# Kernel optimization log

Hardware: AMD Instinct MI355X
Metric: run time of the kernel (lower is better)

## Reference

```python
import jax, jax.numpy as jnp
import numpy as np

N = 20000          # nodes
E = 320000         # edges (avg degree 16)
HID = 256          # hidden_size
HEADS = 8          # num_heads
HD = HID // HEADS  # head_dim = 32


def setup_inputs() -> dict:
    key = jax.random.key(0)
    ks = jax.random.split(key, 12)
    scale = 1.0 / np.sqrt(HID).astype(np.float32)
    def lin_w(k):
        return jax.random.normal(k, (HID, HID), jnp.float32) * scale
    def lin_b(k):
        return jax.random.normal(k, (HID,), jnp.float32) * 0.01
    return {
        "h":   jax.random.normal(ks[0], (N, HID), jnp.float32),
        "Wq": lin_w(ks[1]), "bq": lin_b(ks[2]),
        "Wk": lin_w(ks[3]), "bk": lin_b(ks[4]),
        "Wv": lin_w(ks[5]), "bv": lin_b(ks[6]),
        "Wo": lin_w(ks[7]), "bo": lin_b(ks[8]),
        "rows": jax.random.randint(ks[9],  (E,), 0, N),  # dst/query node of each edge
        "cols": jax.random.randint(ks[10], (E,), 0, N),  # src/key node of each edge
    }


def reference(h, Wq, bq, Wk, bk, Wv, bv, Wo, bo, rows, cols):
    n = h.shape[0]
    scaling = HD ** (-0.5)
    # projections; reshape exactly as torch: (N, head_dim, num_heads)
    q = ((h @ Wq) + bq).reshape(n, HD, HEADS) * scaling
    k = ((h @ Wk) + bk).reshape(n, HD, HEADS)
    v = ((h @ Wv) + bv).reshape(n, HD, HEADS)
    # bsddmm: per-edge, per-head score s[e,h] = sum_d q[rows[e],d,h] * k[cols[e],d,h]
    s = jnp.einsum("edh,edh->eh", q[rows], k[cols])  # [E, HEADS]
    # sparse row-wise softmax (over each row's edges)
    m = jax.ops.segment_max(s, rows, num_segments=n)          # [N, HEADS]
    e = jnp.exp(s - m[rows])                                   # [E, HEADS]
    z = jax.ops.segment_sum(e, rows, num_segments=n)           # [N, HEADS]
    attn = e / z[rows]                                          # [E, HEADS]
    # bspmm: out[i,d,h] = sum_{e: rows[e]=i} attn[e,h] * v[cols[e],d,h]
    out = jax.ops.segment_sum(attn[:, None, :] * v[cols], rows, num_segments=n)  # [N, HD, HEADS]
    return out.reshape(n, -1) @ Wo + bo
```

## Files before the change

### kernel.cpp

```cpp
#include <hip/hip_runtime.h>
#include <hip/hip_bf16.h>
#include <math.h>

#define NNODES 20000
#define NEDGES 320000
#define SCAT_BLOCKS 1250
#define MBLK 313

using f32x4 = __attribute__((ext_vector_type(4))) float;
using s16x8 = __attribute__((ext_vector_type(8))) short;
using u16x8 = __attribute__((ext_vector_type(8))) unsigned short;

__device__ __forceinline__ float bf2f(unsigned short u) {
    union { unsigned int i; float f; } c; c.i = ((unsigned int)u) << 16; return c.f;
}
__device__ __forceinline__ unsigned short f2bf(float f) {
    __hip_bfloat16 h = __float2bfloat16(f);
    return *reinterpret_cast<unsigned short*>(&h);
}
__device__ __forceinline__ u16x8 packA(const float4& x, const float4& y) {
    u16x8 u; u[0]=f2bf(x.x); u[1]=f2bf(x.y); u[2]=f2bf(x.z); u[3]=f2bf(x.w);
             u[4]=f2bf(y.x); u[5]=f2bf(y.y); u[6]=f2bf(y.z); u[7]=f2bf(y.w);
    return u;
}
template <int CTRL>
__device__ __forceinline__ float dpp_xadd(float x) {
    union { float f; int i; } a, b;
    a.f = x;
    b.i = __builtin_amdgcn_update_dpp(0, a.i, CTRL, 0xf, 0xf, true);
    return x + b.f;
}

__global__ __launch_bounds__(256) void prep_hist_k(
    const float* __restrict__ Wq, const float* __restrict__ bq,
    const float* __restrict__ Wk, const float* __restrict__ bk,
    const float* __restrict__ Wv, const float* __restrict__ bv,
    const float* __restrict__ Wo, const int* __restrict__ rows,
    unsigned short* __restrict__ wt, float* __restrict__ bp,
    int* __restrict__ counts)
{
    const int gid = blockIdx.x * 256 + threadIdx.x;
    const float SCQ = 0.17677669529663687f * 1.4426950408889634f;
    if (gid < 262144) {
        const int mat = gid >> 16, r = gid & 65535;
        if (mat < 3) {
            const int k = r >> 8, c = r & 255;
            const int n_old = ((c & 31) << 3) | (c >> 5);
            const float* W = (mat == 0) ? Wq : (mat == 1) ? Wk : Wv;
            float val = W[k * 256 + n_old];
            if (mat == 0) val *= SCQ;
            wt[mat * 65536 + c * 256 + k] = f2bf(val);
        } else {
            const int c = r >> 8, n = r & 255;
            const int n_old = ((c & 31) << 3) | (c >> 5);
            wt[3 * 65536 + n * 256 + c] = f2bf(Wo[n_old * 256 + n]);
        }
    } else if (gid < 262912) {
        const int idx = gid - 262144;
        const int mat = idx >> 8, c = idx & 255;
        const int n_old = ((c & 31) << 3) | (c >> 5);
        const float* b = (mat == 0) ? bq : (mat == 1) ? bk : bv;
        float val = b[n_old];
        if (mat == 0) val *= SCQ;
        bp[mat * 256 + c] = val;
    } else if (gid < 262912 + NEDGES) {
        atomicAdd(&counts[rows[gid - 262912]], 1);
    }
}

__global__ __launch_bounds__(1024) void scan_k(const int* __restrict__ counts,
                                               int* __restrict__ row_start)
{
    __shared__ int wsum[16];
    const int t = threadIdx.x, lane = t & 63, w = t >> 6;
    const int base = t * 20;
    int c[20]; int s = 0;
    #pragma unroll
    for (int j = 0; j < 20; ++j) {
        const int idx = base + j;
        c[j] = (idx < NNODES) ? counts[idx] : 0;
        s += c[j];
    }
    int incl = s;
    #pragma unroll
    for (int off = 1; off < 64; off <<= 1) {
        const int y = __shfl_up(incl, off);
        if (lane >= off) incl += y;
    }
    if (lane == 63) wsum[w] = incl;
    __syncthreads();
    int prev = 0;
    for (int i = 0; i < w; ++i) prev += wsum[i];
    int run = prev + incl - s;
    if (t == 0) row_start[0] = 0;
    #pragma unroll
    for (int j = 0; j < 20; ++j) {
        const int idx = base + j;
        run += c[j];
        if (idx < NNODES) row_start[idx + 1] = run;
    }
}

__global__ __launch_bounds__(256) void qkv_scatter_k(
    const float* __restrict__ h,
    const unsigned short* __restrict__ wt, const float* __restrict__ bp,
    const int* __restrict__ rows, const int* __restrict__ cols,
    const int* __restrict__ row_start, int* __restrict__ cursor,
    int* __restrict__ cols_sorted,
    unsigned short* __restrict__ qo, unsigned short* __restrict__ kv)
{
    const int t = threadIdx.x;
    if (blockIdx.x < SCAT_BLOCKS) {
        const int i = blockIdx.x * 256 + t;
        if (i < NEDGES) {
            const int r = rows[i];
            const int pos = row_start[r] + atomicAdd(&cursor[r], 1);
            cols_sorted[pos] = cols[i];
        }
        return;
    }
    const int bid = blockIdx.x - SCAT_BLOCKS;
    const int mat = bid / MBLK;
    const int bm = (bid % MBLK) * 64;
    const unsigned short* W = wt + mat * 65536;

    __shared__ __align__(16) unsigned short As[64][264];

    const int lane = t & 63, w = t >> 6;
    const int wc = w * 64;
    const int l15 = lane & 15, l4 = lane >> 4;

    u16x8 breg[4][8];
    #pragma unroll
    for (int nt = 0; nt < 4; ++nt)
        #pragma unroll
        for (int k8 = 0; k8 < 8; ++k8)
            breg[nt][k8] = *(const u16x8*)&W[(wc + nt * 16 + l15) * 256 + k8 * 32 + l4 * 8];

    {
        const int arow = t >> 2, acoff = (t & 3) * 8;
        const int m0 = min(bm + arow, NNODES - 1);
        const float* ph = h + m0 * 256 + acoff;
        #pragma unroll
        for (int s = 0; s < 8; ++s) {
            const float4 fa = *(const float4*)(ph + s * 32);
            const float4 fb = *(const float4*)(ph + s * 32 + 4);
            *(u16x8*)&As[arow][acoff + s * 32] = packA(fa, fb);
        }
    }
    __syncthreads();

    f32x4 acc[4][4];
    #pragma unroll
    for (int i = 0; i < 4; ++i)
        #pragma unroll
        for (int j = 0; j < 4; ++j) acc[i][j] = (f32x4){0.f, 0.f, 0.f, 0.f};

    #pragma unroll
    for (int k8 = 0; k8 < 8; ++k8) {
        s16x8 a[4];
        const int kk = k8 * 32 + l4 * 8;
        #pragma unroll
        for (int i = 0; i < 4; ++i)
            a[i] = *(const s16x8*)&As[i * 16 + l15][kk];
        #pragma unroll
        for (int i = 0; i < 4; ++i)
            #pragma unroll
            for (int j = 0; j < 4; ++j)
                acc[i][j] = __builtin_amdgcn_mfma_f32_16x16x32_bf16(
                    a[i], (s16x8)breg[j][k8], acc[i][j], 0, 0, 0);
    }

    #pragma unroll
    for (int j = 0; j < 4; ++j) {
        const int n = wc + j * 16 + l15;
        const float bval = bp[mat * 256 + n];
        const int kvb = ((n >> 3) << 4) + (n & 7) + ((mat == 2) ? 8 : 0);
        #pragma unroll
        for (int i = 0; i < 4; ++i) {
            #pragma unroll
            for (int r = 0; r < 4; ++r) {
                const int m = bm + i * 16 + l4 * 4 + r;
                if (m < NNODES) {
                    const unsigned short val = f2bf(acc[i][j][r] + bval);
                    if (mat == 0) qo[m * 256 + n] = val;
                    else          kv[m * 512 + kvb] = val;
                }
            }
        }
    }
}

__global__ __launch_bounds__(256) void out_proj_k(
    const unsigned short* __restrict__ A,
    const unsigned short* __restrict__ wt, const float* __restrict__ bo,
    float* __restrict__ C)
{
    const int t = threadIdx.x;
    const int bm = blockIdx.x * 64;
    const unsigned short* W = wt + 3 * 65536;

    __shared__ __align__(16) unsigned short As[64][264];

    const int lane = t & 63, w = t >> 6;
    const int wc = w * 64;
    const int l15 = lane & 15, l4 = lane >> 4;

    u16x8 breg[4][8];
    #pragma unroll
    for (int nt = 0; nt < 4; ++nt)
        #pragma unroll
        for (int k8 = 0; k8 < 8; ++k8)
            breg[nt][k8] = *(const u16x8*)&W[(wc + nt * 16 + l15) * 256 + k8 * 32 + l4 * 8];

    {
        const int arow = t >> 2, acoff = (t & 3) * 8;
        const int m0 = min(bm + arow, NNODES - 1);
        const unsigned short* pa = A + m0 * 256 + acoff;
        #pragma unroll
        for (int s = 0; s < 8; ++s)
            *(u16x8*)&As[arow][acoff + s * 32] = *(const u16x8*)(pa + s * 32);
    }
    __syncthreads();

    f32x4 acc[4][4];
    #pragma unroll
    for (int i = 0; i < 4; ++i)
        #pragma unroll
        for (int j = 0; j < 4; ++j) acc[i][j] = (f32x4){0.f, 0.f, 0.f, 0.f};

    #pragma unroll
    for (int k8 = 0; k8 < 8; ++k8) {
        s16x8 a[4];
        const int kk = k8 * 32 + l4 * 8;
        #pragma unroll
        for (int i = 0; i < 4; ++i)
            a[i] = *(const s16x8*)&As[i * 16 + l15][kk];
        #pragma unroll
        for (int i = 0; i < 4; ++i)
            #pragma unroll
            for (int j = 0; j < 4; ++j)
                acc[i][j] = __builtin_amdgcn_mfma_f32_16x16x32_bf16(
                    a[i], (s16x8)breg[j][k8], acc[i][j], 0, 0, 0);
    }

    #pragma unroll
    for (int j = 0; j < 4; ++j) {
        const int n = wc + j * 16 + l15;
        const float bval = bo[n];
        #pragma unroll
        for (int i = 0; i < 4; ++i) {
            #pragma unroll
            for (int r = 0; r < 4; ++r) {
                const int m = bm + i * 16 + l4 * 4 + r;
                if (m < NNODES) C[m * 256 + n] = acc[i][j][r] + bval;
            }
        }
    }
}

__global__ __launch_bounds__(256) void row_attn_k(
    const unsigned short* __restrict__ q, const unsigned short* __restrict__ kv,
    const int* __restrict__ row_start, const int* __restrict__ cols_sorted,
    unsigned short* __restrict__ ot)
{
    const int lane = threadIdx.x & 63;
    const int w5 = lane & 31;
    const int half = lane >> 5;
    const int row = __builtin_amdgcn_readfirstlane(blockIdx.x * 4 + (threadIdx.x >> 6));
    const int rs = row_start[row];
    const int re = row_start[row + 1];
    const int deg = re - rs;

    float qd[8];
    {
        const u16x8 qu = *reinterpret_cast<const u16x8*>(&q[row * 256 + w5 * 8]);
        #pragma unroll
        for (int d = 0; d < 8; ++d) qd[d] = bf2f(qu[d]);
    }
    float o[8] = {0.f, 0.f, 0.f, 0.f, 0.f, 0.f, 0.f, 0.f};
    float z = 0.f;
    const int* cp = cols_sorted + rs;

#define LP(K, V, base) do { \
    const int c0 = cp[min((base), deg - 1)]; \
    const int c1 = cp[min((base) + 1, deg - 1)]; \
    const int cn = half ? c1 : c0; \
    const unsigned short* p_ = kv + cn * 512 + w5 * 16; \
    K = *reinterpret_cast<const u16x8*>(p_); \
    V = *reinterpret_cast<const u16x8*>(p_ + 8); \
} while (0)

#define CMP(K, V, base) do { \
    float pa_ = qd[0] * bf2f(K[0]); \
    float pb_ = qd[1] * bf2f(K[1]); \
    pa_ = fmaf(qd[2], bf2f(K[2]), pa_); \
    pb_ = fmaf(qd[3], bf2f(K[3]), pb_); \
    pa_ = fmaf(qd[4], bf2f(K[4]), pa_); \
    pb_ = fmaf(qd[5], bf2f(K[5]), pb_); \
    pa_ = fmaf(qd[6], bf2f(K[6]), pa_); \
    pb_ = fmaf(qd[7], bf2f(K[7]), pb_); \
    float p_ = pa_ + pb_; \
    p_ = dpp_xadd<0xB1>(p_); \
    p_ = dpp_xadd<0x4E>(p_); \
    const float e_ = ((base) + half < deg) ? exp2f(p_) : 0.f; \
    z += e_; \
    o[0] = fmaf(e_, bf2f(V[0]), o[0]); \
    o[1] = fmaf(e_, bf2f(V[1]), o[1]); \
    o[2] = fmaf(e_, bf2f(V[2]), o[2]); \
    o[3] = fmaf(e_, bf2f(V[3]), o[3]); \
    o[4] = fmaf(e_, bf2f(V[4]), o[4]); \
    o[5] = fmaf(e_, bf2f(V[5]), o[5]); \
    o[6] = fmaf(e_, bf2f(V[6]), o[6]); \
    o[7] = fmaf(e_, bf2f(V[7]), o[7]); \
} while (0)

    if (deg > 0) {
        u16x8 ak0, av0, ak1, av1, bk0, bv0, bk1, bv1;
        LP(ak0, av0, 0);
        LP(ak1, av1, 2);
        for (int i0 = 0; i0 < deg; i0 += 8) {
            const bool hb = (i0 + 4) < deg;
            if (hb) { LP(bk0, bv0, i0 + 4); LP(bk1, bv1, i0 + 6); }
            CMP(ak0, av0, i0);
            CMP(ak1, av1, i0 + 2);
            if (i0 + 8 < deg) { LP(ak0, av0, i0 + 8); LP(ak1, av1, i0 + 10); }
            if (hb) { CMP(bk0, bv0, i0 + 4); CMP(bk1, bv1, i0 + 6); }
        }
    }
#undef LP
#undef CMP

    z += __shfl_xor(z, 32);
    #pragma unroll
    for (int d = 0; d < 8; ++d) o[d] += __shfl_xor(o[d], 32);

    if (half == 0) {
        u16x8 r;
        if (deg > 0) {
            const float iz = 1.0f / z;
            #pragma unroll
            for (int d = 0; d < 8; ++d) r[d] = f2bf(o[d] * iz);
        } else {
            #pragma unroll
            for (int d = 0; d < 8; ++d) r[d] = 0;
        }
        *reinterpret_cast<u16x8*>(&ot[row * 256 + w5 * 8]) = r;
    }
}

extern "C" void kernel_launch(void* const* d_in, const int* in_sizes, int n_in,
                              void* d_out, int out_size, void* d_ws, size_t ws_size,
                              hipStream_t stream)
{
    const float* h  = (const float*)d_in[0];
    const float* Wq = (const float*)d_in[1];
    const float* bq = (const float*)d_in[2];
    const float* Wk = (const float*)d_in[3];
    const float* bk = (const float*)d_in[4];
    const float* Wv = (const float*)d_in[5];
    const float* bv = (const float*)d_in[6];
    const float* Wo = (const float*)d_in[7];
    const float* bo = (const float*)d_in[8];
    const int* rows = (const int*)d_in[9];
    const int* cols = (const int*)d_in[10];
    float* outp = (float*)d_out;

    char* ws = (char*)d_ws;
    unsigned short* q_b  = (unsigned short*)(ws + 0);
    unsigned short* kv_b = (unsigned short*)(ws + 10240000);
    unsigned short* ot_b = (unsigned short*)(ws + 30720000);
    unsigned short* wt   = (unsigned short*)(ws + 40960000);
    float* bp            = (float*)(ws + 41484288);
    int* row_start       = (int*)(ws + 41487360);
    int* counts          = (int*)(ws + 41567488);
    int* cursor          = (int*)(ws + 41647488);
    int* cols_sorted     = (int*)(ws + 41727488);

    hipMemsetAsync(ws + 41567488, 0, 160000, stream);

    prep_hist_k<<<2277, 256, 0, stream>>>(Wq, bq, Wk, bk, Wv, bv, Wo, rows,
                                          wt, bp, counts);
    scan_k<<<1, 1024, 0, stream>>>(counts, row_start);
    qkv_scatter_k<<<SCAT_BLOCKS + 3 * MBLK, 256, 0, stream>>>(
        h, wt, bp, rows, cols, row_start, cursor, cols_sorted, q_b, kv_b);
    row_attn_k<<<5000, 256, 0, stream>>>(q_b, kv_b, row_start, cols_sorted, ot_b);
    out_proj_k<<<MBLK, 256, 0, stream>>>(ot_b, wt, bo, outp);
}
```

Before: 237.1 us.

## Pre-convert h to bf16, retile weights into k-blocked layout, split K/V buffers

The prep kernel now also converts h to bf16 and writes the weights in a k-chunked [mat][k/32][n][32] layout. The GEMM kernels then stream B fragments from global memory per k-step instead of preloading 32 registers of B, which cuts register pressure, and they copy bf16 A tiles directly. K and V are stored in separate 256-wide buffers instead of one interleaved 512-wide buffer, so the attention kernel issues two separate gathers per edge. The cost is an extra 10 MB bf16 write and read of h, plus a shared GEMM body helper.

```diff
diff --git a/kernel.cpp b/kernel.cpp
--- a/kernel.cpp
+++ b/kernel.cpp
@@ -17,11 +17,6 @@
 __device__ __forceinline__ unsigned short f2bf(float f) {
     __hip_bfloat16 h = __float2bfloat16(f);
     return *reinterpret_cast<unsigned short*>(&h);
-}
-__device__ __forceinline__ u16x8 packA(const float4& x, const float4& y) {
-    u16x8 u; u[0]=f2bf(x.x); u[1]=f2bf(x.y); u[2]=f2bf(x.z); u[3]=f2bf(x.w);
-             u[4]=f2bf(y.x); u[5]=f2bf(y.y); u[6]=f2bf(y.z); u[7]=f2bf(y.w);
-    return u;
 }
 template <int CTRL>
 __device__ __forceinline__ float dpp_xadd(float x) {
@@ -31,13 +26,14 @@
     return x + b.f;
 }
 
-__global__ __launch_bounds__(256) void prep_hist_k(
+__global__ __launch_bounds__(256) void prep_all_k(
     const float* __restrict__ Wq, const float* __restrict__ bq,
     const float* __restrict__ Wk, const float* __restrict__ bk,
     const float* __restrict__ Wv, const float* __restrict__ bv,
     const float* __restrict__ Wo, const int* __restrict__ rows,
-    unsigned short* __restrict__ wt, float* __restrict__ bp,
-    int* __restrict__ counts)
+    const float* __restrict__ h,
+    unsigned short* __restrict__ wt2, float* __restrict__ bp,
+    int* __restrict__ counts, unsigned short* __restrict__ hb)
 {
     const int gid = blockIdx.x * 256 + threadIdx.x;
     const float SCQ = 0.17677669529663687f * 1.4426950408889634f;
@@ -49,11 +45,11 @@
             const float* W = (mat == 0) ? Wq : (mat == 1) ? Wk : Wv;
             float val = W[k * 256 + n_old];
             if (mat == 0) val *= SCQ;
-            wt[mat * 65536 + c * 256 + k] = f2bf(val);
+            wt2[((mat * 8 + (k >> 5)) * 256 + c) * 32 + (k & 31)] = f2bf(val);
         } else {
-            const int c = r >> 8, n = r & 255;
-            const int n_old = ((c & 31) << 3) | (c >> 5);
-            wt[3 * 65536 + n * 256 + c] = f2bf(Wo[n_old * 256 + n]);
+            const int k = r & 255, n = r >> 8;
+            const int n_old = ((k & 31) << 3) | (k >> 5);
+            wt2[((24 + (k >> 5)) * 256 + n) * 32 + (k & 31)] = f2bf(Wo[n_old * 256 + n]);
         }
     } else if (gid < 262912) {
         const int idx = gid - 262144;
@@ -63,8 +59,14 @@
         float val = b[n_old];
         if (mat == 0) val *= SCQ;
         bp[mat * 256 + c] = val;
-    } else if (gid < 262912 + NEDGES) {
+    } else if (gid < 582912) {
         atomicAdd(&counts[rows[gid - 262912]], 1);
+    } else {
+        const int i = (gid - 582912) * 4;
+        const float4 f = *reinterpret_cast<const float4*>(&h[i]);
+        ushort4 u;
+        u.x = f2bf(f.x); u.y = f2bf(f.y); u.z = f2bf(f.z); u.w = f2bf(f.w);
+        *reinterpret_cast<ushort4*>(&hb[i]) = u;
     }
 }
 
@@ -101,13 +103,58 @@
     }
 }
 
+__device__ __forceinline__ void gemm_body(
+    const unsigned short* __restrict__ Asrc,
+    const unsigned short* __restrict__ wt2, int mat, int bm,
+    f32x4 (&acc)[4][4], unsigned short (&As)[64][264],
+    int t, int lane)
+{
+    const int l15 = lane & 15, l4 = lane >> 4;
+    const int w = t >> 6;
+    const int wc = w * 64;
+    {
+        const int arow = t >> 2;
+        const int coff = (t & 3) * 64;
+        const int m0 = min(bm + arow, NNODES - 1);
+        const unsigned short* pa = Asrc + m0 * 256 + coff;
+        #pragma unroll
+        for (int s = 0; s < 8; ++s)
+            *(u16x8*)&As[arow][coff + s * 8] = *(const u16x8*)(pa + s * 8);
+    }
+    __syncthreads();
+
+    #pragma unroll
+    for (int i = 0; i < 4; ++i)
+        #pragma unroll
+        for (int j = 0; j < 4; ++j) acc[i][j] = (f32x4){0.f, 0.f, 0.f, 0.f};
+
+    const unsigned short* bb = wt2 + (mat * 8) * 256 * 32 + l4 * 8;
+    #pragma unroll
+    for (int k8 = 0; k8 < 8; ++k8) {
+        s16x8 b[4], a[4];
+        #pragma unroll
+        for (int j = 0; j < 4; ++j)
+            b[j] = *(const s16x8*)(bb + (k8 * 256 + wc + j * 16 + l15) * 32);
+        const int kk = k8 * 32 + l4 * 8;
+        #pragma unroll
+        for (int i = 0; i < 4; ++i)
+            a[i] = *(const s16x8*)&As[i * 16 + l15][kk];
+        #pragma unroll
+        for (int i = 0; i < 4; ++i)
+            #pragma unroll
+            for (int j = 0; j < 4; ++j)
+                acc[i][j] = __builtin_amdgcn_mfma_f32_16x16x32_bf16(a[i], b[j], acc[i][j], 0, 0, 0);
+    }
+}
+
 __global__ __launch_bounds__(256) void qkv_scatter_k(
-    const float* __restrict__ h,
-    const unsigned short* __restrict__ wt, const float* __restrict__ bp,
+    const unsigned short* __restrict__ hb,
+    const unsigned short* __restrict__ wt2, const float* __restrict__ bp,
     const int* __restrict__ rows, const int* __restrict__ cols,
     const int* __restrict__ row_start, int* __restrict__ cursor,
     int* __restrict__ cols_sorted,
-    unsigned short* __restrict__ qo, unsigned short* __restrict__ kv)
+    unsigned short* __restrict__ qo, unsigned short* __restrict__ ko,
+    unsigned short* __restrict__ vo)
 {
     const int t = threadIdx.x;
     if (blockIdx.x < SCAT_BLOCKS) {
@@ -119,73 +166,28 @@
         }
         return;
     }
-    const int bid = blockIdx.x - SCAT_BLOCKS;
-    const int mat = bid / MBLK;
-    const int bm = (bid % MBLK) * 64;
-    const unsigned short* W = wt + mat * 65536;
+    const int gb = blockIdx.x - SCAT_BLOCKS;
+    const int mat = gb / MBLK;
+    const int bm = (gb % MBLK) * 64;
+    unsigned short* outp = (mat == 0) ? qo : (mat == 1) ? ko : vo;
 
     __shared__ __align__(16) unsigned short As[64][264];
-
-    const int lane = t & 63, w = t >> 6;
-    const int wc = w * 64;
+    const int lane = t & 63;
+    f32x4 acc[4][4];
+    gemm_body(hb, wt2, mat, bm, acc, As, t, lane);
+
     const int l15 = lane & 15, l4 = lane >> 4;
-
-    u16x8 breg[4][8];
-    #pragma unroll
-    for (int nt = 0; nt < 4; ++nt)
-        #pragma unroll
-        for (int k8 = 0; k8 < 8; ++k8)
-            breg[nt][k8] = *(const u16x8*)&W[(wc + nt * 16 + l15) * 256 + k8 * 32 + l4 * 8];
-
-    {
-        const int arow = t >> 2, acoff = (t & 3) * 8;
-        const int m0 = min(bm + arow, NNODES - 1);
-        const float* ph = h + m0 * 256 + acoff;
-        #pragma unroll
-        for (int s = 0; s < 8; ++s) {
-            const float4 fa = *(const float4*)(ph + s * 32);
-            const float4 fb = *(const float4*)(ph + s * 32 + 4);
-            *(u16x8*)&As[arow][acoff + s * 32] = packA(fa, fb);
-        }
-    }
-    __syncthreads();
-
-    f32x4 acc[4][4];
-    #pragma unroll
-    for (int i = 0; i < 4; ++i)
-        #pragma unroll
-        for (int j = 0; j < 4; ++j) acc[i][j] = (f32x4){0.f, 0.f, 0.f, 0.f};
-
-    #pragma unroll
-    for (int k8 = 0; k8 < 8; ++k8) {
-        s16x8 a[4];
-        const int kk = k8 * 32 + l4 * 8;
-        #pragma unroll
-        for (int i = 0; i < 4; ++i)
-            a[i] = *(const s16x8*)&As[i * 16 + l15][kk];
-        #pragma unroll
-        for (int i = 0; i < 4; ++i)
-            #pragma unroll
-            for (int j = 0; j < 4; ++j)
-                acc[i][j] = __builtin_amdgcn_mfma_f32_16x16x32_bf16(
-                    a[i], (s16x8)breg[j][k8], acc[i][j], 0, 0, 0);
-    }
-
+    const int wc = (t >> 6) * 64;
     #pragma unroll
     for (int j = 0; j < 4; ++j) {
         const int n = wc + j * 16 + l15;
         const float bval = bp[mat * 256 + n];
-        const int kvb = ((n >> 3) << 4) + (n & 7) + ((mat == 2) ? 8 : 0);
         #pragma unroll
         for (int i = 0; i < 4; ++i) {
             #pragma unroll
             for (int r = 0; r < 4; ++r) {
                 const int m = bm + i * 16 + l4 * 4 + r;
-                if (m < NNODES) {
-                    const unsigned short val = f2bf(acc[i][j][r] + bval);
-                    if (mat == 0) qo[m * 256 + n] = val;
-                    else          kv[m * 512 + kvb] = val;
-                }
+                if (m < NNODES) outp[m * 256 + n] = f2bf(acc[i][j][r] + bval);
             }
         }
     }
@@ -193,57 +195,19 @@
 
 __global__ __launch_bounds__(256) void out_proj_k(
     const unsigned short* __restrict__ A,
-    const unsigned short* __restrict__ wt, const float* __restrict__ bo,
+    const unsigned short* __restrict__ wt2, const float* __restrict__ bo,
     float* __restrict__ C)
 {
     const int t = threadIdx.x;
     const int bm = blockIdx.x * 64;
-    const unsigned short* W = wt + 3 * 65536;
 
     __shared__ __align__(16) unsigned short As[64][264];
-
-    const int lane = t & 63, w = t >> 6;
-    const int wc = w * 64;
+    const int lane = t & 63;
+    f32x4 acc[4][4];
+    gemm_body(A, wt2, 3, bm, acc, As, t, lane);
+
     const int l15 = lane & 15, l4 = lane >> 4;
-
-    u16x8 breg[4][8];
-    #pragma unroll
-    for (int nt = 0; nt < 4; ++nt)
-        #pragma unroll
-        for (int k8 = 0; k8 < 8; ++k8)
-            breg[nt][k8] = *(const u16x8*)&W[(wc + nt * 16 + l15) * 256 + k8 * 32 + l4 * 8];
-
-    {
-        const int arow = t >> 2, acoff = (t & 3) * 8;
-        const int m0 = min(bm + arow, NNODES - 1);
-        const unsigned short* pa = A + m0 * 256 + acoff;
-        #pragma unroll
-        for (int s = 0; s < 8; ++s)
-            *(u16x8*)&As[arow][acoff + s * 32] = *(const u16x8*)(pa + s * 32);
-    }
-    __syncthreads();
-
-    f32x4 acc[4][4];
-    #pragma unroll
-    for (int i = 0; i < 4; ++i)
-        #pragma unroll
-        for (int j = 0; j < 4; ++j) acc[i][j] = (f32x4){0.f, 0.f, 0.f, 0.f};
-
-    #pragma unroll
-    for (int k8 = 0; k8 < 8; ++k8) {
-        s16x8 a[4];
-        const int kk = k8 * 32 + l4 * 8;
-        #pragma unroll
-        for (int i = 0; i < 4; ++i)
-            a[i] = *(const s16x8*)&As[i * 16 + l15][kk];
-        #pragma unroll
-        for (int i = 0; i < 4; ++i)
-            #pragma unroll
-            for (int j = 0; j < 4; ++j)
-                acc[i][j] = __builtin_amdgcn_mfma_f32_16x16x32_bf16(
-                    a[i], (s16x8)breg[j][k8], acc[i][j], 0, 0, 0);
-    }
-
+    const int wc = (t >> 6) * 64;
     #pragma unroll
     for (int j = 0; j < 4; ++j) {
         const int n = wc + j * 16 + l15;
@@ -260,7 +224,8 @@
 }
 
 __global__ __launch_bounds__(256) void row_attn_k(
-    const unsigned short* __restrict__ q, const unsigned short* __restrict__ kv,
+    const unsigned short* __restrict__ q, const unsigned short* __restrict__ kk_,
+    const unsigned short* __restrict__ vv_,
     const int* __restrict__ row_start, const int* __restrict__ cols_sorted,
     unsigned short* __restrict__ ot)
 {
@@ -286,9 +251,8 @@
     const int c0 = cp[min((base), deg - 1)]; \
     const int c1 = cp[min((base) + 1, deg - 1)]; \
     const int cn = half ? c1 : c0; \
-    const unsigned short* p_ = kv + cn * 512 + w5 * 16; \
-    K = *reinterpret_cast<const u16x8*>(p_); \
-    V = *reinterpret_cast<const u16x8*>(p_ + 8); \
+    K = *reinterpret_cast<const u16x8*>(kk_ + cn * 256 + w5 * 8); \
+    V = *reinterpret_cast<const u16x8*>(vv_ + cn * 256 + w5 * 8); \
 } while (0)
 
 #define CMP(K, V, base) do { \
@@ -320,12 +284,12 @@
         LP(ak0, av0, 0);
         LP(ak1, av1, 2);
         for (int i0 = 0; i0 < deg; i0 += 8) {
-            const bool hb = (i0 + 4) < deg;
-            if (hb) { LP(bk0, bv0, i0 + 4); LP(bk1, bv1, i0 + 6); }
+            const bool hb2 = (i0 + 4) < deg;
+            if (hb2) { LP(bk0, bv0, i0 + 4); LP(bk1, bv1, i0 + 6); }
             CMP(ak0, av0, i0);
             CMP(ak1, av1, i0 + 2);
             if (i0 + 8 < deg) { LP(ak0, av0, i0 + 8); LP(ak1, av1, i0 + 10); }
-            if (hb) { CMP(bk0, bv0, i0 + 4); CMP(bk1, bv1, i0 + 6); }
+            if (hb2) { CMP(bk0, bv0, i0 + 4); CMP(bk1, bv1, i0 + 6); }
         }
     }
 #undef LP
@@ -368,22 +332,24 @@
 
     char* ws = (char*)d_ws;
     unsigned short* q_b  = (unsigned short*)(ws + 0);
-    unsigned short* kv_b = (unsigned short*)(ws + 10240000);
+    unsigned short* k_b  = (unsigned short*)(ws + 10240000);
+    unsigned short* v_b  = (unsigned short*)(ws + 20480000);
     unsigned short* ot_b = (unsigned short*)(ws + 30720000);
-    unsigned short* wt   = (unsigned short*)(ws + 40960000);
-    float* bp            = (float*)(ws + 41484288);
-    int* row_start       = (int*)(ws + 41487360);
-    int* counts          = (int*)(ws + 41567488);
-    int* cursor          = (int*)(ws + 41647488);
-    int* cols_sorted     = (int*)(ws + 41727488);
-
-    hipMemsetAsync(ws + 41567488, 0, 160000, stream);
-
-    prep_hist_k<<<2277, 256, 0, stream>>>(Wq, bq, Wk, bk, Wv, bv, Wo, rows,
-                                          wt, bp, counts);
+    unsigned short* h_b  = (unsigned short*)(ws + 40960000);
+    unsigned short* wt2  = (unsigned short*)(ws + 51200000);
+    float* bp            = (float*)(ws + 51724288);
+    int* row_start       = (int*)(ws + 51727360);
+    int* counts          = (int*)(ws + 51807488);
+    int* cursor          = (int*)(ws + 51887488);
+    int* cols_sorted     = (int*)(ws + 51967488);
+
+    hipMemsetAsync(ws + 51807488, 0, 160000, stream);
+
+    prep_all_k<<<7277, 256, 0, stream>>>(Wq, bq, Wk, bk, Wv, bv, Wo, rows, h,
+                                         wt2, bp, counts, h_b);
     scan_k<<<1, 1024, 0, stream>>>(counts, row_start);
     qkv_scatter_k<<<SCAT_BLOCKS + 3 * MBLK, 256, 0, stream>>>(
-        h, wt, bp, rows, cols, row_start, cursor, cols_sorted, q_b, kv_b);
-    row_attn_k<<<5000, 256, 0, stream>>>(q_b, kv_b, row_start, cols_sorted, ot_b);
-    out_proj_k<<<MBLK, 256, 0, stream>>>(ot_b, wt, bo, outp);
-}
+        h_b, wt2, bp, rows, cols, row_start, cursor, cols_sorted, q_b, k_b, v_b);
+    row_attn_k<<<5000, 256, 0, stream>>>(q_b, k_b, v_b, row_start, cols_sorted, ot_b);
+    out_proj_k<<<MBLK, 256, 0, stream>>>(ot_b, wt2, bo, outp);
+}
```

After: 227.2 us. 1.04x faster.
